# Performance work log

Hardware: AMD Instinct MI355X
Metric: run time of the kernel (lower is better)

Reference implementation:

```python
import jax, jax.numpy as jnp
import numpy as np

K = 9  # window half-width (module default k=9)


def _band_edges(N, k):
    # node i connects to all j in [i-k, i+k] \ {i} that are in-range (static band)
    offs = np.concatenate([np.arange(-k, 0), np.arange(1, k + 1)])
    i = np.repeat(np.arange(N), 2 * k)
    j = (np.arange(N)[:, None] + offs[None, :]).reshape(-1)
    mask = (j >= 0) & (j < N)
    return i[mask], j[mask]


def setup_inputs() -> dict:
    key = jax.random.key(0)
    kx, kw, kb = jax.random.split(key, 3)
    B, C, H, W = 8, 256, 64, 64
    x = jax.random.normal(kx, (B, C, H, W), dtype=jnp.float32)
    Wg = jax.random.normal(kw, (C, C), dtype=jnp.float32) * (1.0 / np.float32(np.sqrt(C)))
    b = jax.random.normal(kb, (C,), dtype=jnp.float32) * 0.02
    return {"x": x, "Wg": Wg, "b": b}


def reference(x, Wg, b):
    B, C, H, W = x.shape
    N = H * W
    # faithful replication of the original view/transpose/reshape chain (a real data shuffle)
    x = jnp.transpose(x.reshape(B, C, N), (0, 2, 1)).reshape(B, C, H, W)
    x = jnp.transpose(x.reshape(B, C, N), (0, 2, 1))  # (B, N, C)

    src, dst = _band_edges(N, K)
    # degree WITH self-loop = window size (GCNConv adds self-loops)
    deg = (np.minimum(N, np.arange(N) + K + 1) - np.maximum(0, np.arange(N) - K)).astype(np.float32)
    dinv = jnp.asarray(1.0 / np.sqrt(deg))  # (N,)
    norm = dinv[src] * dinv[dst]            # (E,)

    h = x @ Wg                               # (B, N, C) linear transform (no bias yet)
    m = h[:, src, :] * norm[None, :, None]   # (B, E, C) gathered, normalized messages
    agg = jnp.zeros_like(h).at[:, dst, :].add(m)       # scatter-add to targets
    out = agg + (dinv * dinv)[None, :, None] * h + b   # self-loop term (norm = 1/deg) + bias

    return jnp.transpose(out, (0, 2, 1)).reshape(B, C, H, W)
```

## Files before the change

### kernel.cpp

```cpp
#include <hip/hip_runtime.h>
#include <math.h>

typedef unsigned int uint32;
typedef unsigned short u16;
typedef _Float16 half8 __attribute__((ext_vector_type(8)));
typedef float f32x4 __attribute__((ext_vector_type(4)));

constexpr int NB = 8, NC = 256, NN = 4096;

__device__ __attribute__((aligned(16))) u16 g_xf[NB * NN * NC];
__device__ __attribute__((aligned(16))) u16 g_wf[NC * NC];

__device__ __forceinline__ float dinv_of(int n) {
    int lo = n - 9; lo = lo < 0 ? 0 : lo;
    int hi = n + 9; hi = hi > NN - 1 ? NN - 1 : hi;
    return 1.0f / sqrtf((float)(hi - lo + 1));
}

__device__ __forceinline__ uint32 pkh(float a, float b) {
    _Float16 ha = (_Float16)a, hb = (_Float16)b;
    return (uint32)__builtin_bit_cast(u16, ha) | ((uint32)__builtin_bit_cast(u16, hb) << 16);
}

__device__ __forceinline__ half8 ldh8(const u16* p) {
    return __builtin_bit_cast(half8, *reinterpret_cast<const uint4*>(p));
}

__global__ __launch_bounds__(256) void kprep(const float* __restrict__ x,
                                             const float* __restrict__ wg) {
    const int bid = blockIdx.x, tid = threadIdx.x;
    if (bid < NB * NC) {
        __shared__ float sm[4096];
        const int b = bid >> 8, ch = bid & 255;
        const float4* src = reinterpret_cast<const float4*>(x) + ((size_t)(b * NC + ch) << 10);
        float4* s4 = reinterpret_cast<float4*>(sm);
#pragma unroll
        for (int v = 0; v < 4; ++v) s4[v * 256 + tid] = src[v * 256 + tid];
        __syncthreads();
        const int t = tid & 15, kb2 = tid >> 4;
        const int key = (ch >> 1) & 3;
        u16* row = g_xf + (((size_t)b << 12) + ch + (t << 8)) * NC;
#pragma unroll
        for (int h = 0; h < 2; ++h) {
            const int chunk = kb2 + h * 16;
            uint32 pk[4];
#pragma unroll
            for (int p = 0; p < 4; ++p) {
                float f0 = sm[128 * chunk + 32 * p + t];
                float f1 = sm[128 * chunk + 32 * p + 16 + t];
                pk[p] = pkh(f0, f1);
            }
            const int phys = (chunk & ~3) | ((chunk & 3) ^ key);
            *reinterpret_cast<uint4*>(row + phys * 8) = make_uint4(pk[0], pk[1], pk[2], pk[3]);
        }
    } else {
        __shared__ float sm[32 * 33];
        const int b2 = bid - NB * NC;
        const int k0 = (b2 >> 3) * 32, c0 = (b2 & 7) * 32;
        {
            const int r = tid >> 3, cq = tid & 7;
            float4 v = *reinterpret_cast<const float4*>(wg + (k0 + r) * NC + c0 + cq * 4);
            float* d = sm + r * 33 + cq * 4;
            d[0] = v.x; d[1] = v.y; d[2] = v.z; d[3] = v.w;
        }
        __syncthreads();
        const int c = tid >> 3, kq = tid & 7;
        uint32 o0 = pkh(sm[(kq * 4 + 0) * 33 + c], sm[(kq * 4 + 1) * 33 + c]);
        uint32 o1 = pkh(sm[(kq * 4 + 2) * 33 + c], sm[(kq * 4 + 3) * 33 + c]);
        *reinterpret_cast<uint2*>(g_wf + (c0 + c) * NC + k0 + kq * 4) = make_uint2(o0, o1);
    }
}

__global__ __launch_bounds__(256, 2) void kfuse(const float* __restrict__ bias,
                                                float* __restrict__ out) {
    __shared__ __attribute__((aligned(16))) char smem[43008];
    const int bid = blockIdx.x, tid = threadIdx.x;
    const int b = bid >> 6, ct = (bid >> 5) & 1, nt = bid & 31;
    const int w = tid >> 6, l = tid & 63;
    const int lr = l & 15, lk = l >> 4;
    const int wc0 = ct * 128 + w * 32;
    const int n0 = nt * 128, ne0 = n0 - 16;
    const int koff = (lk ^ ((lr >> 1) & 3)) << 4;

    const int ni = (w < 2) ? 3 : 2;
    const char* gxc = (const char*)g_xf;
    size_t sgb[3]; int sld[3];
#pragma unroll
    for (int ii = 0; ii < 3; ++ii) {
        const int i = w + ii * 4;
        int n = ne0 + i * 16 + (l >> 2);
        n = n < 0 ? 0 : (n > NN - 1 ? NN - 1 : n);
        sgb[ii] = (size_t)((b << 12) + n) * 512 + (l & 3) * 16;
        sld[ii] = i * 1024 + l * 16;
    }

    half8 af[8][2];
#pragma unroll
    for (int s = 0; s < 8; ++s)
#pragma unroll
        for (int cf = 0; cf < 2; ++cf)
            af[s][cf] = ldh8(g_wf + (wc0 + cf * 16 + lr) * NC + s * 32 + lk * 8);

    f32x4 acc[2][10] = {};

#define STAGE(CUR, S)                                                                         \
    _Pragma("unroll")                                                                         \
    for (int ii = 0; ii < 3; ++ii)                                                            \
        if (ii < ni)                                                                          \
            __builtin_amdgcn_global_load_lds(                                                 \
                (const __attribute__((address_space(1))) uint32*)(gxc + sgb[ii] + (S) * 64),  \
                (__attribute__((address_space(3))) uint32*)(smem + (CUR) * 10240 + sld[ii]),  \
                16, 0, 0);

    STAGE(0, 0)
    __syncthreads();
#pragma unroll
    for (int s = 0; s < 8; ++s) {
        const int cur = s & 1;
        if (s < 7) { STAGE(cur ^ 1, s + 1) }
        const char* bb = smem + cur * 10240;
#pragma unroll
        for (int f = 0; f < 10; ++f) {
            half8 bf = *reinterpret_cast<const half8*>(bb + (f * 16 + lr) * 64 + koff);
            acc[0][f] = __builtin_amdgcn_mfma_f32_16x16x32_f16(af[s][0], bf, acc[0][f], 0, 0, 0);
            acc[1][f] = __builtin_amdgcn_mfma_f32_16x16x32_f16(af[s][1], bf, acc[1][f], 0, 0, 0);
        }
        __syncthreads();
    }
#undef STAGE

    char* gsl = smem + w * 10752;
    float dv[10];
#pragma unroll
    for (int f = 0; f < 10; ++f) {
        int n = ne0 + f * 16 + lr;
        dv[f] = (n >= 0 && n < NN) ? dinv_of(n) : 0.f;
    }
#pragma unroll
    for (int cf = 0; cf < 2; ++cf)
#pragma unroll
        for (int f = 0; f < 10; ++f)
#pragma unroll
            for (int v = 0; v < 4; ++v) {
                const int crow = cf * 16 + 4 * lk + v;
                _Float16 hv = (_Float16)(acc[cf][f][v] * dv[f]);
                *(u16*)(gsl + crow * 336 + (f * 16 + lr) * 2) = __builtin_bit_cast(u16, hv);
            }
    __syncthreads();

    half8 ga0v[5], ga1v[5];
#pragma unroll
    for (int KB = 0; KB < 5; ++KB) {
        ga0v[KB] = *reinterpret_cast<const half8*>(gsl + lr * 336 + KB * 64 + lk * 16);
        ga1v[KB] = *reinterpret_cast<const half8*>(gsl + (16 + lr) * 336 + KB * 64 + lk * 16);
    }
    const int dbase = 8 * lk - lr;
    half8 bnv[4];
#pragma unroll
    for (int pt = 0; pt < 4; ++pt) {
        const int off = (pt == 0) ? -16 : (pt == 1) ? 16 : (pt == 2) ? -32 : 0;
#pragma unroll
        for (int jj = 0; jj < 8; ++jj) {
            const int d = dbase + off + jj;
            bnv[pt][jj] = (d >= -9 && d <= 9) ? (_Float16)1.f : (_Float16)0.f;
        }
    }
    f32x4 acc2[2][8] = {};
#pragma unroll
    for (int f = 0; f < 8; ++f)
#pragma unroll
        for (int t = 0; t < 2; ++t) {
            const int KB = (f >> 1) + t;
            const half8 bn = bnv[(f & 1) * 2 + t];
            acc2[0][f] = __builtin_amdgcn_mfma_f32_16x16x32_f16(ga0v[KB], bn, acc2[0][f], 0, 0, 0);
            acc2[1][f] = __builtin_amdgcn_mfma_f32_16x16x32_f16(ga1v[KB], bn, acc2[1][f], 0, 0, 0);
        }

    float dnv[8];
#pragma unroll
    for (int f = 0; f < 8; ++f) dnv[f] = dinv_of(n0 + f * 16 + lr);
#pragma unroll
    for (int cf = 0; cf < 2; ++cf)
#pragma unroll
        for (int v = 0; v < 4; ++v) {
            const int c = wc0 + cf * 16 + 4 * lk + v;
            const float bc = bias[c];
            float* orow = out + (((size_t)(b * NC + c)) << 12) + n0;
#pragma unroll
            for (int f = 0; f < 8; ++f)
                orow[f * 16 + lr] = acc2[cf][f][v] * dnv[f] + bc;
        }
}

extern "C" void kernel_launch(void* const* d_in, const int* in_sizes, int n_in,
                              void* d_out, int out_size, void* d_ws, size_t ws_size,
                              hipStream_t stream) {
    const float* x  = (const float*)d_in[0];
    const float* wg = (const float*)d_in[1];
    const float* bs = (const float*)d_in[2];
    float* out = (float*)d_out;

    hipLaunchKernelGGL(kprep, dim3(NB * NC + 64), dim3(256), 0, stream, x, wg);
    hipLaunchKernelGGL(kfuse, dim3(512), dim3(256), 0, stream, bs, out);
}
```

Measured before the change: 102.7 us.

## Load full x tile into LDS once instead of double-buffered K stages

The fused kernel now issues all global-to-LDS loads for the entire 160-row by 256-channel fp16 tile up front (80 KB of LDS), then runs all 8 K-steps with no per-stage barriers. The global x layout swizzle changes to an XOR over 8 chunks to match the new 512-byte-row LDS read pattern. The per-wave scratch stride for the aggregation stage drops its padding, and one barrier is removed. This removes per-stage synchronisation but gives up overlap between loads and MFMA, and the larger LDS footprint may cut occupancy from the requested two blocks per CU.

```diff
diff --git a/kernel.cpp b/kernel.cpp
--- a/kernel.cpp
+++ b/kernel.cpp
@@ -38,7 +38,7 @@
         for (int v = 0; v < 4; ++v) s4[v * 256 + tid] = src[v * 256 + tid];
         __syncthreads();
         const int t = tid & 15, kb2 = tid >> 4;
-        const int key = (ch >> 1) & 3;
+        const int key = ch & 7;
         u16* row = g_xf + (((size_t)b << 12) + ch + (t << 8)) * NC;
 #pragma unroll
         for (int h = 0; h < 2; ++h) {
@@ -50,48 +50,47 @@
                 float f1 = sm[128 * chunk + 32 * p + 16 + t];
                 pk[p] = pkh(f0, f1);
             }
-            const int phys = (chunk & ~3) | ((chunk & 3) ^ key);
+            const int phys = chunk ^ key;
             *reinterpret_cast<uint4*>(row + phys * 8) = make_uint4(pk[0], pk[1], pk[2], pk[3]);
         }
     } else {
-        __shared__ float sm[32 * 33];
+        __shared__ float sm2[32 * 33];
         const int b2 = bid - NB * NC;
         const int k0 = (b2 >> 3) * 32, c0 = (b2 & 7) * 32;
         {
             const int r = tid >> 3, cq = tid & 7;
             float4 v = *reinterpret_cast<const float4*>(wg + (k0 + r) * NC + c0 + cq * 4);
-            float* d = sm + r * 33 + cq * 4;
+            float* d = sm2 + r * 33 + cq * 4;
             d[0] = v.x; d[1] = v.y; d[2] = v.z; d[3] = v.w;
         }
         __syncthreads();
         const int c = tid >> 3, kq = tid & 7;
-        uint32 o0 = pkh(sm[(kq * 4 + 0) * 33 + c], sm[(kq * 4 + 1) * 33 + c]);
-        uint32 o1 = pkh(sm[(kq * 4 + 2) * 33 + c], sm[(kq * 4 + 3) * 33 + c]);
+        uint32 o0 = pkh(sm2[(kq * 4 + 0) * 33 + c], sm2[(kq * 4 + 1) * 33 + c]);
+        uint32 o1 = pkh(sm2[(kq * 4 + 2) * 33 + c], sm2[(kq * 4 + 3) * 33 + c]);
         *reinterpret_cast<uint2*>(g_wf + (c0 + c) * NC + k0 + kq * 4) = make_uint2(o0, o1);
     }
 }
 
 __global__ __launch_bounds__(256, 2) void kfuse(const float* __restrict__ bias,
                                                 float* __restrict__ out) {
-    __shared__ __attribute__((aligned(16))) char smem[43008];
+    __shared__ __attribute__((aligned(16))) char smem[81920];
     const int bid = blockIdx.x, tid = threadIdx.x;
     const int b = bid >> 6, ct = (bid >> 5) & 1, nt = bid & 31;
     const int w = tid >> 6, l = tid & 63;
     const int lr = l & 15, lk = l >> 4;
     const int wc0 = ct * 128 + w * 32;
     const int n0 = nt * 128, ne0 = n0 - 16;
-    const int koff = (lk ^ ((lr >> 1) & 3)) << 4;
 
-    const int ni = (w < 2) ? 3 : 2;
     const char* gxc = (const char*)g_xf;
-    size_t sgb[3]; int sld[3];
 #pragma unroll
-    for (int ii = 0; ii < 3; ++ii) {
-        const int i = w + ii * 4;
-        int n = ne0 + i * 16 + (l >> 2);
+    for (int ii = 0; ii < 20; ++ii) {
+        const int gi = w * 20 + ii;
+        int n = ne0 + 2 * gi + (l >> 5);
         n = n < 0 ? 0 : (n > NN - 1 ? NN - 1 : n);
-        sgb[ii] = (size_t)((b << 12) + n) * 512 + (l & 3) * 16;
-        sld[ii] = i * 1024 + l * 16;
+        __builtin_amdgcn_global_load_lds(
+            (const __attribute__((address_space(1))) uint32*)(gxc + (size_t)((b << 12) + n) * 512 + (l & 31) * 16),
+            (__attribute__((address_space(3))) uint32*)(smem + gi * 1024 + l * 16),
+            16, 0, 0);
     }
 
     half8 af[8][2];
@@ -101,35 +100,22 @@
         for (int cf = 0; cf < 2; ++cf)
             af[s][cf] = ldh8(g_wf + (wc0 + cf * 16 + lr) * NC + s * 32 + lk * 8);
 
+    __syncthreads();
+
     f32x4 acc[2][10] = {};
-
-#define STAGE(CUR, S)                                                                         \
-    _Pragma("unroll")                                                                         \
-    for (int ii = 0; ii < 3; ++ii)                                                            \
-        if (ii < ni)                                                                          \
-            __builtin_amdgcn_global_load_lds(                                                 \
-                (const __attribute__((address_space(1))) uint32*)(gxc + sgb[ii] + (S) * 64),  \
-                (__attribute__((address_space(3))) uint32*)(smem + (CUR) * 10240 + sld[ii]),  \
-                16, 0, 0);
-
-    STAGE(0, 0)
-    __syncthreads();
 #pragma unroll
     for (int s = 0; s < 8; ++s) {
-        const int cur = s & 1;
-        if (s < 7) { STAGE(cur ^ 1, s + 1) }
-        const char* bb = smem + cur * 10240;
+        const int pbyte = (((4 * s + lk) ^ (lr & 7)) << 4);
 #pragma unroll
         for (int f = 0; f < 10; ++f) {
-            half8 bf = *reinterpret_cast<const half8*>(bb + (f * 16 + lr) * 64 + koff);
+            half8 bf = *reinterpret_cast<const half8*>(smem + (f * 16 + lr) * 512 + pbyte);
             acc[0][f] = __builtin_amdgcn_mfma_f32_16x16x32_f16(af[s][0], bf, acc[0][f], 0, 0, 0);
             acc[1][f] = __builtin_amdgcn_mfma_f32_16x16x32_f16(af[s][1], bf, acc[1][f], 0, 0, 0);
         }
-        __syncthreads();
     }
-#undef STAGE
+    __syncthreads();
 
-    char* gsl = smem + w * 10752;
+    char* gsl = smem + w * 10240;
     float dv[10];
 #pragma unroll
     for (int f = 0; f < 10; ++f) {
@@ -144,15 +130,14 @@
             for (int v = 0; v < 4; ++v) {
                 const int crow = cf * 16 + 4 * lk + v;
                 _Float16 hv = (_Float16)(acc[cf][f][v] * dv[f]);
-                *(u16*)(gsl + crow * 336 + (f * 16 + lr) * 2) = __builtin_bit_cast(u16, hv);
+                *(u16*)(gsl + crow * 320 + (f * 16 + lr) * 2) = __builtin_bit_cast(u16, hv);
             }
-    __syncthreads();
 
     half8 ga0v[5], ga1v[5];
 #pragma unroll
     for (int KB = 0; KB < 5; ++KB) {
-        ga0v[KB] = *reinterpret_cast<const half8*>(gsl + lr * 336 + KB * 64 + lk * 16);
-        ga1v[KB] = *reinterpret_cast<const half8*>(gsl + (16 + lr) * 336 + KB * 64 + lk * 16);
+        ga0v[KB] = *reinterpret_cast<const half8*>(gsl + lr * 320 + KB * 64 + lk * 16);
+        ga1v[KB] = *reinterpret_cast<const half8*>(gsl + (16 + lr) * 320 + KB * 64 + lk * 16);
     }
     const int dbase = 8 * lk - lr;
     half8 bnv[4];
```

Result: no change. 102.4 us (-0.3%).
